# Kernel tuning notes

Measured on AMD Instinct MI355X. Metric: run time of the kernel, lower is better.

The kernel has to match this reference:

```python
import jax, jax.numpy as jnp
import numpy as np


def setup_inputs() -> dict:
    key = jax.random.key(0)
    kq, kv = jax.random.split(key)
    B, Lq, Lv, H = 8, 2048, 2048, 256
    query = jax.random.normal(kq, (B, Lq, H), dtype=jnp.float32)
    value = jax.random.normal(kv, (B, Lv, H), dtype=jnp.float32)
    return {"query": query, "value": value}


def reference(query, value):
    # score[b, q, v] = sum_h query[b, q, h] * value[b, v, h]
    score = jnp.einsum("bqh,bvh->bqv", query, value)
    # softmax over the value axis (last dim), numerically stable
    attn = jax.nn.softmax(score, axis=-1)
    # context[b, q, h] = sum_v attn[b, q, v] * value[b, v, h]
    context = jnp.einsum("bqv,bvh->bqh", attn, value)
    return (context, attn)
```

## Files before the change

### kernel.cpp

```cpp
#include <hip/hip_runtime.h>
#include <hip/hip_bf16.h>

#define LQ 2048
#define LV 2048
#define NH 256
#define NB 8

typedef __attribute__((ext_vector_type(4))) float f32x4;
typedef __attribute__((ext_vector_type(8))) short bf16x8;

__device__ __forceinline__ ushort f32_bf16(float x) {
  union { float f; unsigned u; } c; c.f = x;
  unsigned r = (c.u + 0x7FFFu + ((c.u >> 16) & 1u)) >> 16;
  return (ushort)r;
}
__device__ __forceinline__ float bf16_f32(ushort h) {
  union { unsigned u; float f; } c; c.u = ((unsigned)h) << 16;
  return c.f;
}
__device__ __forceinline__ ushort f32_f16(float x) {
  union { _Float16 h; ushort u; } c; c.h = (_Float16)x; return c.u;
}
__device__ __forceinline__ float f16_f32(ushort u) {
  union { ushort u; _Float16 h; } c; c.u = u; return (float)c.h;
}
__device__ __forceinline__ void gl_lds16(const ushort* g, ushort* l) {
  __builtin_amdgcn_global_load_lds(
      (const __attribute__((address_space(1))) unsigned int*)(g),
      (__attribute__((address_space(3))) unsigned int*)(l), 16, 0, 0);
}


__global__ __launch_bounds__(256) void k_prepQ(
    const float* __restrict__ Q, ushort* __restrict__ Qh, ushort* __restrict__ Ql) {
  int i = blockIdx.x * 256 + threadIdx.x;
  float4 x = reinterpret_cast<const float4*>(Q)[i];
  ushort4 h, l;
  h.x = f32_bf16(x.x); l.x = f32_bf16(x.x - bf16_f32(h.x));
  h.y = f32_bf16(x.y); l.y = f32_bf16(x.y - bf16_f32(h.y));
  h.z = f32_bf16(x.z); l.z = f32_bf16(x.z - bf16_f32(h.z));
  h.w = f32_bf16(x.w); l.w = f32_bf16(x.w - bf16_f32(h.w));
  reinterpret_cast<ushort4*>(Qh)[i] = h;
  reinterpret_cast<ushort4*>(Ql)[i] = l;
}

__global__ __launch_bounds__(256) void k_prepV(
    const float* __restrict__ V, ushort* __restrict__ Vh, ushort* __restrict__ Vl,
    ushort* __restrict__ VhT) {
  int id = blockIdx.x;
  int b = id & 7, vt = (id >> 3) & 31, ht = id >> 8;
  __shared__ ushort sT[64][72];
  int t = threadIdx.x;
  const size_t base = ((size_t)(b * LV) + vt * 64) * NH + ht * 64;
  int r0 = t >> 4, c4 = (t & 15) << 2;
  #pragma unroll
  for (int it = 0; it < 4; ++it) {
    int r = r0 + it * 16;
    size_t off = base + (size_t)r * NH + c4;
    float4 x = *reinterpret_cast<const float4*>(V + off);
    ushort4 h, l;
    h.x = f32_bf16(x.x); l.x = f32_bf16(x.x - bf16_f32(h.x));
    h.y = f32_bf16(x.y); l.y = f32_bf16(x.y - bf16_f32(h.y));
    h.z = f32_bf16(x.z); l.z = f32_bf16(x.z - bf16_f32(h.z));
    h.w = f32_bf16(x.w); l.w = f32_bf16(x.w - bf16_f32(h.w));
    *reinterpret_cast<ushort4*>(Vh + off) = h;
    *reinterpret_cast<ushort4*>(Vl + off) = l;
    *reinterpret_cast<ushort4*>(&sT[r][c4]) = h;
  }
  __syncthreads();
  int hh = t & 63, vc = t >> 6;
  ushort tmp[16];
  #pragma unroll
  for (int j = 0; j < 16; ++j) tmp[j] = sT[vc * 16 + j][hh];
  ushort* dst = VhT + ((size_t)(b * NH) + ht * 64 + hh) * LV + vt * 64 + vc * 16;
  *reinterpret_cast<ushort4*>(dst)      = *reinterpret_cast<ushort4*>(&tmp[0]);
  *reinterpret_cast<ushort4*>(dst + 4)  = *reinterpret_cast<ushort4*>(&tmp[4]);
  *reinterpret_cast<ushort4*>(dst + 8)  = *reinterpret_cast<ushort4*>(&tmp[8]);
  *reinterpret_cast<ushort4*>(dst + 12) = *reinterpret_cast<ushort4*>(&tmp[12]);
}

__global__ __launch_bounds__(512) void k_scores7(
    const ushort* __restrict__ Qh, const ushort* __restrict__ Ql,
    const ushort* __restrict__ Vh, const ushort* __restrict__ Vl,
    float* __restrict__ S, float2* __restrict__ PS) {
  extern __shared__ ushort dynlds[];
  int id = blockIdx.x;
  int b = id & 7, qt = (id >> 3) & 7, vt = id >> 6;
  int t = threadIdx.x, lane = t & 63, w = t >> 6;

  const size_t bq = (size_t)(b * LQ) + qt * 256;
  const size_t bv = (size_t)(b * LV) + vt * 256;

#define LBASE(buf, arr) ((char*)dynlds + ((buf) * 4 + (arr)) * (256 * 64))

#define STAGE(buf, kt)                                                      \
  {                                                                         \
    int krow = t >> 2, c = t & 3;                                           \
    _Pragma("unroll")                                                       \
    for (int hh = 0; hh < 2; ++hh) {                                        \
      int row = hh * 128 + krow;                                            \
      int csrc = c ^ ((row >> 1) & 3);                                      \
      size_t gq = (bq + row) * NH + (kt) * 32 + csrc * 8;                   \
      size_t gv = (bv + row) * NH + (kt) * 32 + csrc * 8;                   \
      gl_lds16(Qh + gq, (ushort*)(LBASE(buf, 0) + row * 64 + c * 16));      \
      gl_lds16(Ql + gq, (ushort*)(LBASE(buf, 1) + row * 64 + c * 16));      \
      gl_lds16(Vh + gv, (ushort*)(LBASE(buf, 2) + row * 64 + c * 16));      \
      gl_lds16(Vl + gv, (ushort*)(LBASE(buf, 3) + row * 64 + c * 16));      \
    }                                                                       \
  }

  int wq = w >> 1, wv = w & 1;
  int ar = wq * 64 + (lane & 15);
  int br = wv * 128 + (lane & 15);
  int kb = lane >> 4;

  f32x4 acc[4][8] = {};

  STAGE(0, 0);
  STAGE(1, 1);

  #pragma unroll
  for (int kt = 0; kt < 8; ++kt) {
    const int cur = kt & 1;
    if (kt < 7) { asm volatile("s_waitcnt vmcnt(8)" ::: "memory"); }
    else        { asm volatile("s_waitcnt vmcnt(0)" ::: "memory"); }
    __builtin_amdgcn_sched_barrier(0);
    __builtin_amdgcn_s_barrier();
    __builtin_amdgcn_sched_barrier(0);

    bf16x8 ah[4], al[4];
    #pragma unroll
    for (int m = 0; m < 4; ++m) {
      int r = ar + m * 16;
      int off = r * 64 + ((kb ^ ((r >> 1) & 3)) << 4);
      ah[m] = *reinterpret_cast<const bf16x8*>(LBASE(cur, 0) + off);
      al[m] = *reinterpret_cast<const bf16x8*>(LBASE(cur, 1) + off);
    }
    __builtin_amdgcn_s_setprio(1);
    #pragma unroll
    for (int n = 0; n < 8; ++n) {
      int r = br + n * 16;
      int off = r * 64 + ((kb ^ ((r >> 1) & 3)) << 4);
      bf16x8 bh = *reinterpret_cast<const bf16x8*>(LBASE(cur, 2) + off);
      bf16x8 bl = *reinterpret_cast<const bf16x8*>(LBASE(cur, 3) + off);
      #pragma unroll
      for (int m = 0; m < 4; ++m) {
        acc[m][n] = __builtin_amdgcn_mfma_f32_16x16x32_bf16(ah[m], bh, acc[m][n], 0, 0, 0);
        acc[m][n] = __builtin_amdgcn_mfma_f32_16x16x32_bf16(ah[m], bl, acc[m][n], 0, 0, 0);
        acc[m][n] = __builtin_amdgcn_mfma_f32_16x16x32_bf16(al[m], bh, acc[m][n], 0, 0, 0);
      }
    }
    __builtin_amdgcn_s_setprio(0);
    __builtin_amdgcn_sched_barrier(0);
    __builtin_amdgcn_s_barrier();
    __builtin_amdgcn_sched_barrier(0);
    if (kt < 6) STAGE(cur, kt + 2);
  }

  const int g = lane >> 4, c0 = lane & 15;
  #pragma unroll
  for (int m = 0; m < 4; ++m) {
    #pragma unroll
    for (int j = 0; j < 4; ++j) {
      float mx = acc[m][0][j];
      #pragma unroll
      for (int n = 1; n < 8; ++n) mx = fmaxf(mx, acc[m][n][j]);
      #pragma unroll
      for (int off = 1; off < 16; off <<= 1) mx = fmaxf(mx, __shfl_xor(mx, off));
      float e[8];
      float s = 0.f;
      #pragma unroll
      for (int n = 0; n < 8; ++n) { e[n] = __expf(acc[m][n][j] - mx); s += e[n]; }
      #pragma unroll
      for (int off = 1; off < 16; off <<= 1) s += __shfl_xor(s, off);
      int row = qt * 256 + wq * 64 + m * 16 + g * 4 + j;
      if (c0 == 0) {
        float2 v; v.x = mx; v.y = s;
        PS[((size_t)(b * LQ) + row) * 16 + vt * 2 + wv] = v;
      }
      ushort* pr = (ushort*)(S + ((size_t)(b * LQ) + row) * LV + 1024);
      int cb = vt * 256 + wv * 128 + c0;
      #pragma unroll
      for (int n = 0; n < 8; ++n) pr[cb + n * 16] = f32_f16(e[n]);
    }
  }
#undef STAGE
#undef LBASE
}

__global__ __launch_bounds__(512) void k_ctx10(
    const ushort* __restrict__ VhT, const float2* __restrict__ PS,
    float* __restrict__ A, float* __restrict__ C) {
  int id = blockIdx.x;
  int b = id & 7, qs = id >> 3;
  __shared__ float lf[32][16];
  __shared__ __align__(16) ushort sP[4][32 * 64];

  int t = threadIdx.x, lane = t & 63, w = t >> 6;
  float* Ab = A + (size_t)b * LQ * LV + (size_t)qs * 32 * LV;
  const ushort* Vb = VhT + (size_t)b * NH * LV;

  const int prow = t >> 4, pc = (t & 15) << 2;
  float* aaddr = Ab + (size_t)prow * LV + pc;
  const ushort* a16 = (const ushort*)(Ab + (size_t)prow * LV + 1024) + pc;
  const int poff = (prow * 128 + pc * 2) ^ ((prow & 7) << 4);

  {
    int row = t >> 4, seg = t & 15;
    float2 p = PS[((size_t)(b * LQ) + qs * 32 + row) * 16 + seg];
    float M = p.x, s = p.y;
    #pragma unroll
    for (int off = 1; off < 16; off <<= 1) {
      float mo = __shfl_xor(M, off), so = __shfl_xor(s, off);
      float mn = fmaxf(M, mo);
      s = s * __expf(M - mn) + so * __expf(mo - mn);
      M = mn;
    }
    lf[row][seg] = __expf(p.x - M) / s;
  }
  __syncthreads();

#define PRODUCE(xv, v0, buf, fac)                                           \
  {                                                                         \
    float4 p;                                                               \
    p.x = f16_f32((xv).x) * (fac); p.y = f16_f32((xv).y) * (fac);           \
    p.z = f16_f32((xv).z) * (fac); p.w = f16_f32((xv).w) * (fac);           \
    *reinterpret_cast<float4*>(aaddr + (v0)) = p;                           \
    ushort4 pk;                                                             \
    pk.x = f32_bf16(p.x); pk.y = f32_bf16(p.y);                             \
    pk.z = f32_bf16(p.z); pk.w = f32_bf16(p.w);                             \
    *reinterpret_cast<ushort4*>((char*)&sP[buf][0] + poff) = pk;            \
  }

  ushort4 x0 = *reinterpret_cast<const ushort4*>(a16);
  ushort4 x1 = *reinterpret_cast<const ushort4*>(a16 + 64);
  {
    float f0 = lf[prow][0];
    PRODUCE(x0, 0, 0, f0);
    PRODUCE(x1, 64, 1, f0);
  }
  x0 = *reinterpret_cast<const ushort4*>(a16 + 128);
  x1 = *reinterpret_cast<const ushort4*>(a16 + 192);
  __syncthreads();

  f32x4 acc[2][2] = {};
  const int NP = LV / 128;

  for (int p = 0; p < NP; ++p) {
    const int cur = (p & 1) << 1;
    const int nxt = cur ^ 2;
    const int v0 = p * 128;
    if (p + 1 < NP) {
      float fn = lf[prow][p + 1];
      PRODUCE(x0, v0 + 128, nxt, fn);
      PRODUCE(x1, v0 + 192, nxt + 1, fn);
    }
    if (p + 2 < NP) {
      x0 = *reinterpret_cast<const ushort4*>(a16 + v0 + 256);
      x1 = *reinterpret_cast<const ushort4*>(a16 + v0 + 320);
    }

    #pragma unroll
    for (int c = 0; c < 2; ++c) {
      #pragma unroll
      for (int ks = 0; ks < 2; ++ks) {
        int vbyte = ks * 64 + ((lane >> 4) << 4);
        bf16x8 pa[2];
        #pragma unroll
        for (int i2 = 0; i2 < 2; ++i2) {
          int arow = i2 * 16 + (lane & 15);
          pa[i2] = *reinterpret_cast<const bf16x8*>(
              (char*)&sP[cur + c][0] + ((arow * 128 + vbyte) ^ ((arow & 7) << 4)));
        }
        #pragma unroll
        for (int n = 0; n < 2; ++n) {
          int hrow = w * 32 + n * 16 + (lane & 15);
          bf16x8 vb = *reinterpret_cast<const bf16x8*>(
              Vb + (size_t)hrow * LV + v0 + c * 64 + ks * 32 + ((lane >> 4) << 3));
          #pragma unroll
          for (int i2 = 0; i2 < 2; ++i2)
            acc[i2][n] = __builtin_amdgcn_mfma_f32_16x16x32_bf16(pa[i2], vb, acc[i2][n], 0, 0, 0);
        }
      }
    }
    __syncthreads();
  }
#undef PRODUCE

  float* Cb = C + ((size_t)b * LQ + qs * 32) * NH + w * 32;
  int rb = (lane >> 4) << 2, c0 = lane & 15;
  #pragma unroll
  for (int i2 = 0; i2 < 2; ++i2)
    #pragma unroll
    for (int j = 0; j < 4; ++j)
      #pragma unroll
      for (int n = 0; n < 2; ++n)
        Cb[(size_t)(i2 * 16 + rb + j) * NH + n * 16 + c0] = acc[i2][n][j];
}


__global__ __launch_bounds__(256) void k_scores_fb(
    const float* __restrict__ Q, const float* __restrict__ V,
    float* __restrict__ S) {
  int id = blockIdx.x;
  int b = id & 7;
  int inner = id >> 3;
  int qt = inner & 31;
  int vt = inner >> 5;
  __shared__ ushort sQh[64 * 64], sQl[64 * 64], sVh[64 * 64], sVl[64 * 64];
  const float* Qb = Q + (size_t)(b * LQ + qt * 64) * NH;
  const float* Vb = V + (size_t)(b * LV + vt * 64) * NH;
  const int t = threadIdx.x;
  const int lane = t & 63;
  const int w = t >> 6;
  f32x4 acc[4] = {};
  const int row0 = t >> 4;
  const int col4 = (t & 15) << 2;
  for (int kc = 0; kc < 4; ++kc) {
    #pragma unroll
    for (int it = 0; it < 4; ++it) {
      int row = row0 + (it << 4);
      const float4 qx = *reinterpret_cast<const float4*>(Qb + (size_t)row * NH + kc * 64 + col4);
      const float4 vx = *reinterpret_cast<const float4*>(Vb + (size_t)row * NH + kc * 64 + col4);
      int off = ((row * 128 + col4 * 2) ^ ((row & 7) << 4)) >> 1;
      ushort4 h, l;
      h.x = f32_bf16(qx.x); l.x = f32_bf16(qx.x - bf16_f32(h.x));
      h.y = f32_bf16(qx.y); l.y = f32_bf16(qx.y - bf16_f32(h.y));
      h.z = f32_bf16(qx.z); l.z = f32_bf16(qx.z - bf16_f32(h.z));
      h.w = f32_bf16(qx.w); l.w = f32_bf16(qx.w - bf16_f32(h.w));
      *reinterpret_cast<ushort4*>(&sQh[off]) = h;
      *reinterpret_cast<ushort4*>(&sQl[off]) = l;
      h.x = f32_bf16(vx.x); l.x = f32_bf16(vx.x - bf16_f32(h.x));
      h.y = f32_bf16(vx.y); l.y = f32_bf16(vx.y - bf16_f32(h.y));
      h.z = f32_bf16(vx.z); l.z = f32_bf16(vx.z - bf16_f32(h.z));
      h.w = f32_bf16(vx.w); l.w = f32_bf16(vx.w - bf16_f32(h.w));
      *reinterpret_cast<ushort4*>(&sVh[off]) = h;
      *reinterpret_cast<ushort4*>(&sVl[off]) = l;
    }
    __syncthreads();
    int arow = (w << 4) + (lane & 15);
    int abase = arow * 128;
    int aswz = (arow & 7) << 4;
    #pragma unroll
    for (int ks = 0; ks < 2; ++ks) {
      int koffB = (ks << 6) + ((lane >> 4) << 4);
      int aoff = ((abase + koffB) ^ aswz) >> 1;
      bf16x8 ah = *reinterpret_cast<const bf16x8*>(&sQh[aoff]);
      bf16x8 al = *reinterpret_cast<const bf16x8*>(&sQl[aoff]);
      #pragma unroll
      for (int n = 0; n < 4; ++n) {
        int brow = (n << 4) + (lane & 15);
        int boff = (((brow * 128) + koffB) ^ ((brow & 7) << 4)) >> 1;
        bf16x8 bh = *reinterpret_cast<const bf16x8*>(&sVh[boff]);
        bf16x8 bl = *reinterpret_cast<const bf16x8*>(&sVl[boff]);
        acc[n] = __builtin_amdgcn_mfma_f32_16x16x32_bf16(ah, bh, acc[n], 0, 0, 0);
        acc[n] = __builtin_amdgcn_mfma_f32_16x16x32_bf16(ah, bl, acc[n], 0, 0, 0);
        acc[n] = __builtin_amdgcn_mfma_f32_16x16x32_bf16(al, bh, acc[n], 0, 0, 0);
      }
    }
    __syncthreads();
  }
  float* Sp = S + (size_t)b * LQ * LV + (size_t)(qt * 64) * LV + vt * 64;
  int rbase = (w << 4) + ((lane >> 4) << 2);
  int c0 = lane & 15;
  #pragma unroll
  for (int n = 0; n < 4; ++n)
    #pragma unroll
    for (int j = 0; j < 4; ++j)
      Sp[(size_t)(rbase + j) * LV + (n << 4) + c0] = acc[n][j];
}

__global__ __launch_bounds__(256) void k_stats_fb(const float* __restrict__ S,
                                                  float* __restrict__ ml) {
  const size_t r = blockIdx.x;
  const float* row = S + r * LV;
  int t = threadIdx.x;
  float4 a = *reinterpret_cast<const float4*>(row + (t << 2));
  float4 c = *reinterpret_cast<const float4*>(row + 1024 + (t << 2));
  float m = fmaxf(fmaxf(fmaxf(a.x, a.y), fmaxf(a.z, a.w)),
                  fmaxf(fmaxf(c.x, c.y), fmaxf(c.z, c.w)));
  #pragma unroll
  for (int off = 32; off; off >>= 1) m = fmaxf(m, __shfl_xor(m, off));
  __shared__ float redm[4];
  __shared__ float reds[4];
  if ((t & 63) == 0) redm[t >> 6] = m;
  __syncthreads();
  m = fmaxf(fmaxf(redm[0], redm[1]), fmaxf(redm[2], redm[3]));
  float s = __expf(a.x - m) + __expf(a.y - m) + __expf(a.z - m) + __expf(a.w - m)
          + __expf(c.x - m) + __expf(c.y - m) + __expf(c.z - m) + __expf(c.w - m);
  #pragma unroll
  for (int off = 32; off; off >>= 1) s += __shfl_xor(s, off);
  if ((t & 63) == 0) reds[t >> 6] = s;
  __syncthreads();
  if (t == 0) {
    float tot = reds[0] + reds[1] + reds[2] + reds[3];
    ml[2 * r] = m;
    ml[2 * r + 1] = 1.0f / tot;
  }
}

__global__ __launch_bounds__(256) void k_ctx_fb(
    const float* __restrict__ V, const float* __restrict__ ml,
    float* __restrict__ A, float* __restrict__ C) {
  int id = blockIdx.x;
  int b = id & 7;
  int qt = id >> 3;
  __shared__ ushort sP[32 * 40];
  __shared__ ushort sVT[256 * 40];
  __shared__ float lmv[32], liv[32];
  int t = threadIdx.x;
  int lane = t & 63;
  int w = t >> 6;
  int wr = w >> 1, wh = w & 1;
  if (t < 32) {
    size_t r = (size_t)b * LQ + qt * 32 + t;
    lmv[t] = ml[2 * r];
    liv[t] = ml[2 * r + 1];
  }
  __syncthreads();
  f32x4 acc[8] = {};
  float* Ab = A + (size_t)b * LQ * LV + (size_t)(qt * 32) * LV;
  const float* Vb = V + (size_t)b * LV * NH;
  const int prow = t >> 3;
  const int pv4 = (t & 7) << 2;
  for (int v0 = 0; v0 < LV; v0 += 32) {
    {
      float* addr = Ab + (size_t)prow * LV + v0 + pv4;
      float4 s4 = *reinterpret_cast<const float4*>(addr);
      float m = lmv[prow], inv = liv[prow];
      float4 p4;
      p4.x = __expf(s4.x - m) * inv;
      p4.y = __expf(s4.y - m) * inv;
      p4.z = __expf(s4.z - m) * inv;
      p4.w = __expf(s4.w - m) * inv;
      *reinterpret_cast<float4*>(addr) = p4;
      ushort4 pb;
      pb.x = f32_bf16(p4.x); pb.y = f32_bf16(p4.y);
      pb.z = f32_bf16(p4.z); pb.w = f32_bf16(p4.w);
      *reinterpret_cast<ushort4*>(&sP[prow * 40 + pv4]) = pb;
    }
    #pragma unroll 4
    for (int vl = 0; vl < 32; ++vl) {
      float x = Vb[(size_t)(v0 + vl) * NH + t];
      sVT[t * 40 + vl] = f32_bf16(x);
    }
    __syncthreads();
    bf16x8 pa = *reinterpret_cast<const bf16x8*>(
        &sP[((wr << 4) + (lane & 15)) * 40 + ((lane >> 4) << 3)]);
    #pragma unroll
    for (int n = 0; n < 8; ++n) {
      int hrow = (wh << 7) + (n << 4) + (lane & 15);
      bf16x8 vb = *reinterpret_cast<const bf16x8*>(
          &sVT[hrow * 40 + ((lane >> 4) << 3)]);
      acc[n] = __builtin_amdgcn_mfma_f32_16x16x32_bf16(pa, vb, acc[n], 0, 0, 0);
    }
    __syncthreads();
  }
  float* Cb = C + ((size_t)b * LQ + qt * 32) * NH;
  int rbase = (wr << 4) + ((lane >> 4) << 2);
  int c0 = lane & 15;
  #pragma unroll
  for (int n = 0; n < 8; ++n)
    #pragma unroll
    for (int j = 0; j < 4; ++j)
      Cb[(size_t)(rbase + j) * NH + (wh << 7) + (n << 4) + c0] = acc[n][j];
}


extern "C" void kernel_launch(void* const* d_in, const int* in_sizes, int n_in,
                              void* d_out, int out_size, void* d_ws, size_t ws_size,
                              hipStream_t stream) {
  const float* Q = (const float*)d_in[0];
  const float* V = (const float*)d_in[1];
  float* out = (float*)d_out;
  float* C = out;
  float* A = out + (size_t)NB * LQ * NH;

  const size_t NE = (size_t)NB * LQ * NH;
  const size_t PSN = (size_t)NB * LQ * 16;
  const size_t need = NE * 2 * 5 + PSN * 8;
  const int DYN_LDS = 2 * 4 * 256 * 32 * 2;

  bool big_lds_ok =
      hipFuncSetAttribute((const void*)k_scores7,
                          hipFuncAttributeMaxDynamicSharedMemorySize,
                          DYN_LDS) == hipSuccess;

  if (ws_size >= need && big_lds_ok) {
    ushort* Qh  = (ushort*)d_ws;
    ushort* Ql  = Qh + NE;
    ushort* Vh  = Ql + NE;
    ushort* Vl  = Vh + NE;
    ushort* VhT = Vl + NE;
    float2* PS  = (float2*)(VhT + NE);
    k_prepQ<<<dim3(NE / 4 / 256), dim3(256), 0, stream>>>(Q, Qh, Ql);
    k_prepV<<<dim3(NB * 32 * 4), dim3(256), 0, stream>>>(V, Vh, Vl, VhT);
    k_scores7<<<dim3(NB * 8 * 8), dim3(512), DYN_LDS, stream>>>(Qh, Ql, Vh, Vl, A, PS);
    k_ctx10<<<dim3(NB * 64), dim3(512), 0, stream>>>(VhT, PS, A, C);
  } else {
    float* ml = (float*)d_ws;
    k_scores_fb<<<dim3(NB * 32 * 32), dim3(256), 0, stream>>>(Q, V, A);
    k_stats_fb<<<dim3(NB * LQ), dim3(256), 0, stream>>>(A, ml);
    k_ctx_fb<<<dim3(NB * 64), dim3(256), 0, stream>>>(V, ml, A, C);
  }
}
```

Measured before the change: 146.8 us.

## Switch split-precision score GEMM from 3-term bf16 to 2-term fp16

```diff
diff --git a/kernel.cpp b/kernel.cpp
--- a/kernel.cpp
+++ b/kernel.cpp
@@ -8,6 +8,7 @@
 
 typedef __attribute__((ext_vector_type(4))) float f32x4;
 typedef __attribute__((ext_vector_type(8))) short bf16x8;
+typedef __attribute__((ext_vector_type(8))) _Float16 f16x8;
 
 __device__ __forceinline__ ushort f32_bf16(float x) {
   union { float f; unsigned u; } c; c.f = x;
@@ -31,22 +32,21 @@
 }
 
 
-__global__ __launch_bounds__(256) void k_prepQ(
+__global__ __launch_bounds__(256) void k_prepQ2(
     const float* __restrict__ Q, ushort* __restrict__ Qh, ushort* __restrict__ Ql) {
   int i = blockIdx.x * 256 + threadIdx.x;
   float4 x = reinterpret_cast<const float4*>(Q)[i];
   ushort4 h, l;
-  h.x = f32_bf16(x.x); l.x = f32_bf16(x.x - bf16_f32(h.x));
-  h.y = f32_bf16(x.y); l.y = f32_bf16(x.y - bf16_f32(h.y));
-  h.z = f32_bf16(x.z); l.z = f32_bf16(x.z - bf16_f32(h.z));
-  h.w = f32_bf16(x.w); l.w = f32_bf16(x.w - bf16_f32(h.w));
+  h.x = f32_f16(x.x); l.x = f32_f16(x.x - f16_f32(h.x));
+  h.y = f32_f16(x.y); l.y = f32_f16(x.y - f16_f32(h.y));
+  h.z = f32_f16(x.z); l.z = f32_f16(x.z - f16_f32(h.z));
+  h.w = f32_f16(x.w); l.w = f32_f16(x.w - f16_f32(h.w));
   reinterpret_cast<ushort4*>(Qh)[i] = h;
   reinterpret_cast<ushort4*>(Ql)[i] = l;
 }
 
-__global__ __launch_bounds__(256) void k_prepV(
-    const float* __restrict__ V, ushort* __restrict__ Vh, ushort* __restrict__ Vl,
-    ushort* __restrict__ VhT) {
+__global__ __launch_bounds__(256) void k_prepV2(
+    const float* __restrict__ V, ushort* __restrict__ Vf, ushort* __restrict__ VfT) {
   int id = blockIdx.x;
   int b = id & 7, vt = (id >> 3) & 31, ht = id >> 8;
   __shared__ ushort sT[64][72];
@@ -58,13 +58,10 @@
     int r = r0 + it * 16;
     size_t off = base + (size_t)r * NH + c4;
     float4 x = *reinterpret_cast<const float4*>(V + off);
-    ushort4 h, l;
-    h.x = f32_bf16(x.x); l.x = f32_bf16(x.x - bf16_f32(h.x));
-    h.y = f32_bf16(x.y); l.y = f32_bf16(x.y - bf16_f32(h.y));
-    h.z = f32_bf16(x.z); l.z = f32_bf16(x.z - bf16_f32(h.z));
-    h.w = f32_bf16(x.w); l.w = f32_bf16(x.w - bf16_f32(h.w));
-    *reinterpret_cast<ushort4*>(Vh + off) = h;
-    *reinterpret_cast<ushort4*>(Vl + off) = l;
+    ushort4 h;
+    h.x = f32_f16(x.x); h.y = f32_f16(x.y);
+    h.z = f32_f16(x.z); h.w = f32_f16(x.w);
+    *reinterpret_cast<ushort4*>(Vf + off) = h;
     *reinterpret_cast<ushort4*>(&sT[r][c4]) = h;
   }
   __syncthreads();
@@ -72,16 +69,16 @@
   ushort tmp[16];
   #pragma unroll
   for (int j = 0; j < 16; ++j) tmp[j] = sT[vc * 16 + j][hh];
-  ushort* dst = VhT + ((size_t)(b * NH) + ht * 64 + hh) * LV + vt * 64 + vc * 16;
+  ushort* dst = VfT + ((size_t)(b * NH) + ht * 64 + hh) * LV + vt * 64 + vc * 16;
   *reinterpret_cast<ushort4*>(dst)      = *reinterpret_cast<ushort4*>(&tmp[0]);
   *reinterpret_cast<ushort4*>(dst + 4)  = *reinterpret_cast<ushort4*>(&tmp[4]);
   *reinterpret_cast<ushort4*>(dst + 8)  = *reinterpret_cast<ushort4*>(&tmp[8]);
   *reinterpret_cast<ushort4*>(dst + 12) = *reinterpret_cast<ushort4*>(&tmp[12]);
 }
 
-__global__ __launch_bounds__(512) void k_scores7(
+__global__ __launch_bounds__(512) void k_scores8(
     const ushort* __restrict__ Qh, const ushort* __restrict__ Ql,
-    const ushort* __restrict__ Vh, const ushort* __restrict__ Vl,
+    const ushort* __restrict__ Vf,
     float* __restrict__ S, float2* __restrict__ PS) {
   extern __shared__ ushort dynlds[];
   int id = blockIdx.x;
@@ -91,7 +88,7 @@
   const size_t bq = (size_t)(b * LQ) + qt * 256;
   const size_t bv = (size_t)(b * LV) + vt * 256;
 
-#define LBASE(buf, arr) ((char*)dynlds + ((buf) * 4 + (arr)) * (256 * 64))
+#define LBASE(buf, arr) ((char*)dynlds + ((buf) * 3 + (arr)) * (256 * 64))
 
 #define STAGE(buf, kt)                                                      \
   {                                                                         \
@@ -104,8 +101,7 @@
       size_t gv = (bv + row) * NH + (kt) * 32 + csrc * 8;                   \
       gl_lds16(Qh + gq, (ushort*)(LBASE(buf, 0) + row * 64 + c * 16));      \
       gl_lds16(Ql + gq, (ushort*)(LBASE(buf, 1) + row * 64 + c * 16));      \
-      gl_lds16(Vh + gv, (ushort*)(LBASE(buf, 2) + row * 64 + c * 16));      \
-      gl_lds16(Vl + gv, (ushort*)(LBASE(buf, 3) + row * 64 + c * 16));      \
+      gl_lds16(Vf + gv, (ushort*)(LBASE(buf, 2) + row * 64 + c * 16));      \
     }                                                                       \
   }
 
@@ -122,32 +118,30 @@
   #pragma unroll
   for (int kt = 0; kt < 8; ++kt) {
     const int cur = kt & 1;
-    if (kt < 7) { asm volatile("s_waitcnt vmcnt(8)" ::: "memory"); }
+    if (kt < 7) { asm volatile("s_waitcnt vmcnt(6)" ::: "memory"); }
     else        { asm volatile("s_waitcnt vmcnt(0)" ::: "memory"); }
     __builtin_amdgcn_sched_barrier(0);
     __builtin_amdgcn_s_barrier();
     __builtin_amdgcn_sched_barrier(0);
 
-    bf16x8 ah[4], al[4];
+    f16x8 ah[4], al[4];
     #pragma unroll
     for (int m = 0; m < 4; ++m) {
       int r = ar + m * 16;
       int off = r * 64 + ((kb ^ ((r >> 1) & 3)) << 4);
-      ah[m] = *reinterpret_cast<const bf16x8*>(LBASE(cur, 0) + off);
-      al[m] = *reinterpret_cast<const bf16x8*>(LBASE(cur, 1) + off);
+      ah[m] = *reinterpret_cast<const f16x8*>(LBASE(cur, 0) + off);
+      al[m] = *reinterpret_cast<const f16x8*>(LBASE(cur, 1) + off);
     }
     __builtin_amdgcn_s_setprio(1);
     #pragma unroll
     for (int n = 0; n < 8; ++n) {
       int r = br + n * 16;
       int off = r * 64 + ((kb ^ ((r >> 1) & 3)) << 4);
-      bf16x8 bh = *reinterpret_cast<const bf16x8*>(LBASE(cur, 2) + off);
-      bf16x8 bl = *reinterpret_cast<const bf16x8*>(LBASE(cur, 3) + off);
+      f16x8 bf = *reinterpret_cast<const f16x8*>(LBASE(cur, 2) + off);
       #pragma unroll
       for (int m = 0; m < 4; ++m) {
-        acc[m][n] = __builtin_amdgcn_mfma_f32_16x16x32_bf16(ah[m], bh, acc[m][n], 0, 0, 0);
-        acc[m][n] = __builtin_amdgcn_mfma_f32_16x16x32_bf16(ah[m], bl, acc[m][n], 0, 0, 0);
-        acc[m][n] = __builtin_amdgcn_mfma_f32_16x16x32_bf16(al[m], bh, acc[m][n], 0, 0, 0);
+        acc[m][n] = __builtin_amdgcn_mfma_f32_16x16x32_f16(ah[m], bf, acc[m][n], 0, 0, 0);
+        acc[m][n] = __builtin_amdgcn_mfma_f32_16x16x32_f16(al[m], bf, acc[m][n], 0, 0, 0);
       }
     }
     __builtin_amdgcn_s_setprio(0);
@@ -188,8 +182,8 @@
 #undef LBASE
 }
 
-__global__ __launch_bounds__(512) void k_ctx10(
-    const ushort* __restrict__ VhT, const float2* __restrict__ PS,
+__global__ __launch_bounds__(512) void k_ctx11(
+    const ushort* __restrict__ VfT, const float2* __restrict__ PS,
     float* __restrict__ A, float* __restrict__ C) {
   int id = blockIdx.x;
   int b = id & 7, qs = id >> 3;
@@ -198,7 +192,7 @@
 
   int t = threadIdx.x, lane = t & 63, w = t >> 6;
   float* Ab = A + (size_t)b * LQ * LV + (size_t)qs * 32 * LV;
-  const ushort* Vb = VhT + (size_t)b * NH * LV;
+  const ushort* Vb = VfT + (size_t)b * NH * LV;
 
   const int prow = t >> 4, pc = (t & 15) << 2;
   float* aaddr = Ab + (size_t)prow * LV + pc;
@@ -227,8 +221,8 @@
     p.z = f16_f32((xv).z) * (fac); p.w = f16_f32((xv).w) * (fac);           \
     *reinterpret_cast<float4*>(aaddr + (v0)) = p;                           \
     ushort4 pk;                                                             \
-    pk.x = f32_bf16(p.x); pk.y = f32_bf16(p.y);                             \
-    pk.z = f32_bf16(p.z); pk.w = f32_bf16(p.w);                             \
+    pk.x = f32_f16(p.x); pk.y = f32_f16(p.y);                               \
+    pk.z = f32_f16(p.z); pk.w = f32_f16(p.w);                               \
     *reinterpret_cast<ushort4*>((char*)&sP[buf][0] + poff) = pk;            \
   }
 
@@ -265,21 +259,21 @@
       #pragma unroll
       for (int ks = 0; ks < 2; ++ks) {
         int vbyte = ks * 64 + ((lane >> 4) << 4);
-        bf16x8 pa[2];
+        f16x8 pa[2];
         #pragma unroll
         for (int i2 = 0; i2 < 2; ++i2) {
           int arow = i2 * 16 + (lane & 15);
-          pa[i2] = *reinterpret_cast<const bf16x8*>(
+          pa[i2] = *reinterpret_cast<const f16x8*>(
               (char*)&sP[cur + c][0] + ((arow * 128 + vbyte) ^ ((arow & 7) << 4)));
         }
         #pragma unroll
         for (int n = 0; n < 2; ++n) {
           int hrow = w * 32 + n * 16 + (lane & 15);
-          bf16x8 vb = *reinterpret_cast<const bf16x8*>(
+          f16x8 vb = *reinterpret_cast<const f16x8*>(
               Vb + (size_t)hrow * LV + v0 + c * 64 + ks * 32 + ((lane >> 4) << 3));
           #pragma unroll
           for (int i2 = 0; i2 < 2; ++i2)
-            acc[i2][n] = __builtin_amdgcn_mfma_f32_16x16x32_bf16(pa[i2], vb, acc[i2][n], 0, 0, 0);
+            acc[i2][n] = __builtin_amdgcn_mfma_f32_16x16x32_f16(pa[i2], vb, acc[i2][n], 0, 0, 0);
         }
       }
     }
@@ -478,25 +472,24 @@
 
   const size_t NE = (size_t)NB * LQ * NH;
   const size_t PSN = (size_t)NB * LQ * 16;
-  const size_t need = NE * 2 * 5 + PSN * 8;
-  const int DYN_LDS = 2 * 4 * 256 * 32 * 2;
+  const size_t need = NE * 2 * 4 + PSN * 8;
+  const int DYN_LDS = 2 * 3 * 256 * 64;
 
   bool big_lds_ok =
-      hipFuncSetAttribute((const void*)k_scores7,
+      hipFuncSetAttribute((const void*)k_scores8,
                           hipFuncAttributeMaxDynamicSharedMemorySize,
                           DYN_LDS) == hipSuccess;
 
   if (ws_size >= need && big_lds_ok) {
     ushort* Qh  = (ushort*)d_ws;
     ushort* Ql  = Qh + NE;
-    ushort* Vh  = Ql + NE;
-    ushort* Vl  = Vh + NE;
-    ushort* VhT = Vl + NE;
-    float2* PS  = (float2*)(VhT + NE);
-    k_prepQ<<<dim3(NE / 4 / 256), dim3(256), 0, stream>>>(Q, Qh, Ql);
-    k_prepV<<<dim3(NB * 32 * 4), dim3(256), 0, stream>>>(V, Vh, Vl, VhT);
-    k_scores7<<<dim3(NB * 8 * 8), dim3(512), DYN_LDS, stream>>>(Qh, Ql, Vh, Vl, A, PS);
-    k_ctx10<<<dim3(NB * 64), dim3(512), 0, stream>>>(VhT, PS, A, C);
+    ushort* Vf  = Ql + NE;
+    ushort* VfT = Vf + NE;
+    float2* PS  = (float2*)(VfT + NE);
+    k_prepQ2<<<dim3(NE / 4 / 256), dim3(256), 0, stream>>>(Q, Qh, Ql);
+    k_prepV2<<<dim3(NB * 32 * 4), dim3(256), 0, stream>>>(V, Vf, VfT);
+    k_scores8<<<dim3(NB * 8 * 8), dim3(512), DYN_LDS, stream>>>(Qh, Ql, Vf, A, PS);
+    k_ctx11<<<dim3(NB * 64), dim3(512), 0, stream>>>(VfT, PS, A, C);
   } else {
     float* ml = (float*)d_ws;
     k_scores_fb<<<dim3(NB * 32 * 32), dim3(256), 0, stream>>>(Q, V, A);
```

Result: faster. 136.6 us (-7.0%).
